# Optimization experiments

Hardware: AMD Instinct MI355X
Metric: run time of the kernel (lower is better)

## Reference

```python
import jax, jax.numpy as jnp
import numpy as np

D_MODEL = 1024
N_LAYERS = 2
D_STATE = 64
D_CONV = 4
EXPAND = 2
D_INNER = EXPAND * D_MODEL            # 2048
HEADDIM = D_STATE                     # 64 (headdim=d_state per module code)
NHEADS = D_INNER // HEADDIM           # 32
CONV_DIM = D_INNER + 2 * D_STATE      # 2176 (ngroups=1)
D_IN_PROJ = 2 * D_INNER + 2 * D_STATE + NHEADS  # 4256
EPS = 1e-5


def setup_inputs() -> dict:
    key = jax.random.key(0)
    ks = jax.random.split(key, 8)
    B, L = 2, 4096
    return {
        "x": jax.random.normal(ks[0], (B, L, D_MODEL), jnp.float32),
        "ln_w": jnp.ones((N_LAYERS, D_MODEL), jnp.float32),
        "ln_b": jnp.zeros((N_LAYERS, D_MODEL), jnp.float32),
        "in_proj_w": jax.random.normal(ks[1], (N_LAYERS, D_IN_PROJ, D_MODEL), jnp.float32) * (D_MODEL ** -0.5),
        "conv_w": jax.random.normal(ks[2], (N_LAYERS, CONV_DIM, D_CONV), jnp.float32) * (D_CONV ** -0.5),
        "conv_b": jnp.zeros((N_LAYERS, CONV_DIM), jnp.float32),
        "dt_bias": jax.random.normal(ks[3], (N_LAYERS, NHEADS), jnp.float32) * 0.5,
        "A_log": jnp.log(jax.random.uniform(ks[4], (N_LAYERS, NHEADS), jnp.float32, 1.0, 16.0)),
        "D": jnp.ones((N_LAYERS, NHEADS), jnp.float32),
        "rms_w": jnp.ones((N_LAYERS, D_INNER), jnp.float32),
        "out_proj_w": jax.random.normal(ks[5], (N_LAYERS, D_MODEL, D_INNER), jnp.float32) * (D_INNER ** -0.5),
    }


def _layernorm(x, w, b):
    m = x.mean(-1, keepdims=True)
    v = ((x - m) ** 2).mean(-1, keepdims=True)
    return (x - m) * jax.lax.rsqrt(v + EPS) * w + b


def _mamba2(u, in_w, conv_w, conv_b, dt_bias, A_log, Dp, rms_w, out_w):
    b, l, _ = u.shape
    zxbcdt = u @ in_w.T                                   # (b,l,D_IN_PROJ)
    z, xBC, dt = jnp.split(zxbcdt, [D_INNER, D_INNER + CONV_DIM], axis=-1)
    dt = jax.nn.softplus(dt + dt_bias)                    # (b,l,H)
    # causal depthwise conv over sequence
    xBC = jnp.transpose(xBC, (0, 2, 1))                   # (b,C,l)
    xBC = jax.lax.conv_general_dilated(
        xBC, conv_w[:, None, :], (1,), [(D_CONV - 1, 0)],
        dimension_numbers=("NCH", "OIH", "NCH"), feature_group_count=CONV_DIM)
    xBC = jnp.transpose(xBC, (0, 2, 1)) + conv_b
    xBC = jax.nn.silu(xBC)
    xh, Bm, Cm = jnp.split(xBC, [D_INNER, D_INNER + D_STATE], axis=-1)
    xh = xh.reshape(b, l, NHEADS, HEADDIM)                # (b,l,H,P)
    A = -jnp.exp(A_log)                                   # (H,)
    dA = jnp.exp(dt * A)                                  # (b,l,H)

    def step(state, inputs):
        dA_t, dt_t, x_t, B_t, C_t = inputs                # (b,H),(b,H),(b,H,P),(b,N),(b,N)
        state = dA_t[:, :, None, None] * state + (dt_t[:, :, None] * x_t)[..., None] * B_t[:, None, None, :]
        y_t = jnp.einsum("bhpn,bn->bhp", state, C_t)
        return state, y_t

    xs = (jnp.moveaxis(dA, 1, 0), jnp.moveaxis(dt, 1, 0), jnp.moveaxis(xh, 1, 0),
          jnp.moveaxis(Bm, 1, 0), jnp.moveaxis(Cm, 1, 0))
    init = jnp.zeros((b, NHEADS, HEADDIM, D_STATE), u.dtype)
    _, ys = jax.lax.scan(step, init, xs)                  # ys: (l,b,H,P)
    y = jnp.moveaxis(ys, 0, 1) + Dp[None, None, :, None] * xh
    y = y.reshape(b, l, D_INNER)
    # gated RMSNorm (norm_before_gate=False): gate then rmsnorm
    y = y * jax.nn.silu(z)
    y = y * jax.lax.rsqrt(jnp.mean(y * y, -1, keepdims=True) + EPS) * rms_w
    return y @ out_w.T


def reference(x, ln_w, ln_b, in_proj_w, conv_w, conv_b, dt_bias, A_log, D, rms_w, out_proj_w):
    h = x
    for i in range(N_LAYERS):
        res = h
        h = _layernorm(h, ln_w[i], ln_b[i])
        h = _mamba2(h, in_proj_w[i], conv_w[i], conv_b[i], dt_bias[i], A_log[i], D[i], rms_w[i], out_proj_w[i])
        h = h + res
    return h
```

## Files before the change

kernel.cpp:

```cpp
#include <hip/hip_runtime.h>
#include <stdint.h>

#define D_MODEL   1024
#define D_STATE   64
#define D_INNER   2048
#define NHEADS    32
#define CONV_DIM  2176
#define D_IN_PROJ 4256
#define NPAD1     4352
#define LSEQ      4096
#define BL        8192
#define NCHUNK    32
#define TCH       128
#define EPS       1e-5f

typedef __attribute__((ext_vector_type(8))) _Float16 f16x8;
typedef __attribute__((ext_vector_type(4))) _Float16 f16x4;
typedef __attribute__((ext_vector_type(4))) float f32x4;

__device__ __forceinline__ void load_lds16(const void* g, void* l) {
  __builtin_amdgcn_global_load_lds((const __attribute__((address_space(1))) void*)g,
                                   (__attribute__((address_space(3))) void*)l, 16, 0, 0);
}

__global__ __launch_bounds__(256) void cvt_w1_kernel(const float* __restrict__ w,
                                                     _Float16* __restrict__ o) {
  size_t idx = (size_t)blockIdx.x * 256 + threadIdx.x;
  int k = idx & 1023;
  size_t nr = idx >> 10;
  int layer = (int)(nr / NPAD1);
  int n = (int)(nr % NPAD1);
  float v = (n < D_IN_PROJ) ? w[((size_t)layer * D_IN_PROJ + n) * 1024 + k] : 0.f;
  o[idx] = (_Float16)v;
}
__global__ __launch_bounds__(256) void cvt_w2_kernel(const float* __restrict__ w,
                                                     _Float16* __restrict__ o) {
  size_t idx = (size_t)blockIdx.x * 256 + threadIdx.x;
  o[idx] = (_Float16)w[idx];
}

__global__ __launch_bounds__(256) void ln_kernel(const float* __restrict__ x,
                                                 const float* __restrict__ w,
                                                 const float* __restrict__ b,
                                                 _Float16* __restrict__ o) {
  int row = blockIdx.x, tid = threadIdx.x;
  const float* xr = x + (size_t)row * D_MODEL;
  float4 v = *(const float4*)(xr + tid * 4);
  float s = v.x + v.y + v.z + v.w;
  float q = v.x * v.x + v.y * v.y + v.z * v.z + v.w * v.w;
  for (int off = 1; off < 64; off <<= 1) { s += __shfl_xor(s, off); q += __shfl_xor(q, off); }
  __shared__ float rs[4], rq[4];
  int wave = tid >> 6, lane = tid & 63;
  if (lane == 0) { rs[wave] = s; rq[wave] = q; }
  __syncthreads();
  s = rs[0] + rs[1] + rs[2] + rs[3];
  q = rq[0] + rq[1] + rq[2] + rq[3];
  float mean = s * (1.f / D_MODEL);
  float var = q * (1.f / D_MODEL) - mean * mean;
  float rstd = rsqrtf(var + EPS);
  int c = tid * 4;
  f16x4 ov;
  ov[0] = (_Float16)((v.x - mean) * rstd * w[c + 0] + b[c + 0]);
  ov[1] = (_Float16)((v.y - mean) * rstd * w[c + 1] + b[c + 1]);
  ov[2] = (_Float16)((v.z - mean) * rstd * w[c + 2] + b[c + 2]);
  ov[3] = (_Float16)((v.w - mean) * rstd * w[c + 3] + b[c + 3]);
  *(f16x4*)(o + (size_t)row * D_MODEL + c) = ov;
}

template <int MODE>
__global__ __launch_bounds__(512, 4) void gemm_f16_kernel(
    const _Float16* __restrict__ A, int lda,
    const _Float16* __restrict__ Bw, int K, int NBN,
    _Float16* __restrict__ Zb, _Float16* __restrict__ XPRE, float* __restrict__ AUX,
    float* __restrict__ Cf, const float* __restrict__ resid) {
  __shared__ _Float16 lA[3][256 * 32];
  __shared__ _Float16 lB[3][128 * 32];
  int tid = threadIdx.x;
  int wv = tid >> 6, lane = tid & 63;
  int nwg = gridDim.x;
  int cpx = nwg >> 3;
  int wg = ((int)blockIdx.x & 7) * cpx + ((int)blockIdx.x >> 3);
  int band = wg / (4 * NBN), rem = wg % (4 * NBN);
  int bm = band * 4 + (rem & 3);
  int bn = rem >> 2;

  const int wm = (wv >> 1) * 64, wn = (wv & 1) * 64;
  const int fr = lane & 15;
  const int s4 = lane >> 4;
  size_t aoff = (size_t)(bm * 256) * lda;
  size_t boff = (size_t)(bn * 128) * K;

  f32x4 acc[4][4];
  f32x4 zero = {0.f, 0.f, 0.f, 0.f};
#pragma unroll
  for (int i = 0; i < 4; ++i)
#pragma unroll
    for (int j = 0; j < 4; ++j) acc[i][j] = zero;

  auto stage = [&](int k0, int buf) {
#pragma unroll
    for (int c = 0; c < 2; ++c) {
      int row = (wv * 2 + c) * 16 + (lane >> 2);
      int col = k0 + (((lane & 3) ^ ((row >> 1) & 3)) << 3);
      load_lds16(A + aoff + (size_t)row * lda + col,
                 &lA[buf][(wv * 2 + c) * 512 + lane * 8]);
    }
    int rowb = wv * 16 + (lane >> 2);
    int colb = k0 + (((lane & 3) ^ ((rowb >> 1) & 3)) << 3);
    load_lds16(Bw + boff + (size_t)rowb * K + colb, &lB[buf][wv * 512 + lane * 8]);
  };

  int nk = K >> 5;
  stage(0, 0);
  stage(32, 1);
  int cur = 0;
  for (int kk = 0; kk < nk; ++kk) {
    if (kk + 2 < nk) {
      int sb = cur + 2; if (sb >= 3) sb -= 3;
      stage((kk + 2) << 5, sb);
      asm volatile("s_waitcnt vmcnt(6)" ::: "memory");
    } else if (kk + 1 < nk) {
      asm volatile("s_waitcnt vmcnt(3)" ::: "memory");
    } else {
      asm volatile("s_waitcnt vmcnt(0)" ::: "memory");
    }
    __builtin_amdgcn_s_barrier();
    __builtin_amdgcn_sched_barrier(0);
    f16x8 af[4], bf[4];
#pragma unroll
    for (int i = 0; i < 4; ++i) {
      int R = wm + i * 16 + fr;
      af[i] = *(const f16x8*)&lA[cur][R * 32 + ((s4 ^ ((R >> 1) & 3)) << 3)];
    }
#pragma unroll
    for (int j = 0; j < 4; ++j) {
      int R = wn + j * 16 + fr;
      bf[j] = *(const f16x8*)&lB[cur][R * 32 + ((s4 ^ ((R >> 1) & 3)) << 3)];
    }
#pragma unroll
    for (int i = 0; i < 4; ++i)
#pragma unroll
      for (int j = 0; j < 4; ++j)
        acc[i][j] = __builtin_amdgcn_mfma_f32_16x16x32_f16(af[i], bf[j], acc[i][j], 0, 0, 0);
    __builtin_amdgcn_sched_barrier(0);
    __builtin_amdgcn_s_barrier();
    cur = cur + 1; if (cur >= 3) cur = 0;
  }

  int r0 = (lane >> 4) * 4;
  int cc = lane & 15;
#pragma unroll
  for (int i = 0; i < 4; ++i) {
#pragma unroll
    for (int j = 0; j < 4; ++j) {
      int col = bn * 128 + wn + j * 16 + cc;
#pragma unroll
      for (int r = 0; r < 4; ++r) {
        size_t row = (size_t)(bm * 256 + wm + i * 16 + r0 + r);
        float v = acc[i][j][r];
        if constexpr (MODE == 0) {
          if (col < 2048)       Zb[row * 2048 + col] = (_Float16)v;
          else if (col < 4096)  XPRE[row * 2048 + (col - 2048)] = (_Float16)v;
          else if (col < 4256)  AUX[row * 160 + (col - 4096)] = v;
        } else {
          size_t idx = row * 1024 + col;
          Cf[idx] = v + resid[idx];
        }
      }
    }
  }
}

__global__ __launch_bounds__(128) void dtlc_kernel(const float* __restrict__ aux,
                                                   const float* __restrict__ dtb,
                                                   const float* __restrict__ alog,
                                                   float* __restrict__ dtt,
                                                   float* __restrict__ lco) {
  int bid = blockIdx.x;
  int h = bid >> 6, b = (bid >> 5) & 1, ct = bid & 31;
  int tid = threadIdx.x, lane = tid & 63;
  int l = b * LSEQ + ct * TCH + tid;
  float A = -__expf(alog[h]);
  float v = aux[(size_t)l * 160 + 128 + h] + dtb[h];
  float sp = (v > 20.f) ? v : log1pf(expf(v));
  size_t base = (size_t)h * BL + b * LSEQ + ct * TCH;
  dtt[base + tid] = sp;
  float d = sp * A;
#pragma unroll
  for (int off = 1; off < 64; off <<= 1) {
    float o = __shfl_up(d, off);
    if (lane >= off) d += o;
  }
  __shared__ float tot;
  if (tid == 63) tot = d;
  __syncthreads();
  if (tid >= 64) d += tot;
  lco[base + tid] = d;
}

__global__ __launch_bounds__(256) void conv_kernel(const _Float16* __restrict__ xpre,
                                                   const float* __restrict__ aux,
                                                   const float* __restrict__ cw,
                                                   const float* __restrict__ cb,
                                                   _Float16* __restrict__ xt,
                                                   float* __restrict__ Bo,
                                                   float* __restrict__ Co,
                                                   _Float16* __restrict__ bt) {
  int c = blockIdx.y * 256 + threadIdx.x;
  if (c >= CONV_DIM) return;
  int l0 = blockIdx.x * 16;
  float w0 = cw[c * 4 + 0], w1 = cw[c * 4 + 1], w2 = cw[c * 4 + 2], w3 = cw[c * 4 + 3];
  float bias = cb[c];
  bool isx = (c < 2048);
  auto ldx = [&](int l) -> float {
    return isx ? (float)xpre[(size_t)l * 2048 + c] : aux[(size_t)l * 160 + (c - 2048)];
  };
  float a0 = 0.f, a1 = 0.f, a2 = 0.f;
  if ((l0 & 4095) != 0) { a0 = ldx(l0 - 3); a1 = ldx(l0 - 2); a2 = ldx(l0 - 1); }
  _Float16 ob[16];
#pragma unroll
  for (int t = 0; t < 16; ++t) {
    int l = l0 + t;
    float a3 = ldx(l);
    float acc = bias + a0 * w0 + a1 * w1 + a2 * w2 + a3 * w3;
    acc = acc / (1.f + __expf(-acc));
    ob[t] = (_Float16)acc;
    if (!isx) {
      if (c < 2112) Bo[(size_t)l * 64 + (c - 2048)] = acc;
      else          Co[(size_t)l * 64 + (c - 2112)] = acc;
    }
    a0 = a1; a1 = a2; a2 = a3;
  }
  f16x8 v0, v1;
#pragma unroll
  for (int j = 0; j < 8; ++j) { v0[j] = ob[j]; v1[j] = ob[8 + j]; }
  if (isx) {
    *(f16x8*)&xt[(size_t)c * 8192 + l0] = v0;
    *(f16x8*)&xt[(size_t)c * 8192 + l0 + 8] = v1;
  } else if (c < 2112) {
    *(f16x8*)&bt[(size_t)(c - 2048) * 8192 + l0] = v0;
    *(f16x8*)&bt[(size_t)(c - 2048) * 8192 + l0 + 8] = v1;
  }
}

__global__ __launch_bounds__(256) void scan_state_kernel(
    const _Float16* __restrict__ xt, const _Float16* __restrict__ bt,
    const float* __restrict__ lc, const float* __restrict__ dtt,
    float* __restrict__ cs) {
  int bid = blockIdx.x;
  int chunk = bid & 31, h = (bid >> 5) & 31, b = bid >> 10;
  int tid = threadIdx.x;
  size_t gb = (size_t)b * LSEQ + chunk * TCH;
  size_t cdb = (size_t)h * BL + gb;
  __shared__ _Float16 xtl[64 * 128];
  __shared__ _Float16 btl[64 * 128];
  __shared__ float ldsW[128];
  if (tid < 128) ldsW[tid] = dtt[cdb + tid] * __expf(lc[cdb + 127] - lc[cdb + tid]);
  __syncthreads();
  int rr = tid >> 4, cl = tid & 15;
#pragma unroll
  for (int p = 0; p < 4; ++p) {
    int row = p * 16 + rr;
    f16x8 v = *(const f16x8*)&xt[(size_t)(h * 64 + row) * BL + gb + cl * 8];
    f16x8 bv = *(const f16x8*)&bt[(size_t)row * BL + gb + cl * 8];
    f16x8 sv;
#pragma unroll
    for (int j = 0; j < 8; ++j) sv[j] = (_Float16)((float)v[j] * ldsW[cl * 8 + j]);
    int byo = (row * 256 + cl * 16) ^ ((row & 7) << 4);
    *(f16x8*)((char*)xtl + byo) = sv;
    *(f16x8*)((char*)btl + byo) = bv;
  }
  __syncthreads();
  int wv = tid >> 6, lane = tid & 63;
  int fr = lane & 15, fk = (lane >> 4) * 8, r0 = (lane >> 4) * 4, cc = lane & 15;
  int swz = (fr & 7) << 4;
  f32x4 acc[4];
  f32x4 zero = {0.f, 0.f, 0.f, 0.f};
#pragma unroll
  for (int j = 0; j < 4; ++j) acc[j] = zero;
#pragma unroll
  for (int k0 = 0; k0 < 128; k0 += 32) {
    f16x8 af = *(const f16x8*)((char*)xtl + (((wv * 16 + fr) * 256 + (k0 + fk) * 2) ^ swz));
#pragma unroll
    for (int j = 0; j < 4; ++j) {
      f16x8 bf = *(const f16x8*)((char*)btl + (((j * 16 + fr) * 256 + (k0 + fk) * 2) ^ swz));
      acc[j] = __builtin_amdgcn_mfma_f32_16x16x32_f16(af, bf, acc[j], 0, 0, 0);
    }
  }
  size_t cbase = (((size_t)(b * 32 + h) * 32) + chunk) * 4096;
#pragma unroll
  for (int j = 0; j < 4; ++j)
#pragma unroll
    for (int r = 0; r < 4; ++r)
      cs[cbase + (wv * 16 + r0 + r) * 64 + j * 16 + cc] = acc[j][r];
}

__global__ __launch_bounds__(256) void scan_p2_kernel(float* __restrict__ cs,
                                                      const float* __restrict__ lc) {
  int bid = blockIdx.x;
  int b = bid >> 7, h = (bid >> 2) & 31, pq = bid & 3;
  int tid = threadIdx.x;
  size_t base = ((size_t)(b * 32 + h) * 32) * 4096 + (size_t)(pq * 256 + tid) * 4;
  const float* lcd = lc + (size_t)h * BL + b * LSEQ;
  float4 s = {0.f, 0.f, 0.f, 0.f};
  for (int c = 0; c < NCHUNK; ++c) {
    size_t idx = base + (size_t)c * 4096;
    float4 e = *(const float4*)&cs[idx];
    float P = __expf(lcd[c * TCH + TCH - 1]);
    *(float4*)&cs[idx] = s;
    s.x = e.x + P * s.x;
    s.y = e.y + P * s.y;
    s.z = e.z + P * s.z;
    s.w = e.w + P * s.w;
  }
}

__global__ __launch_bounds__(256) void scan_y_kernel(
    const _Float16* __restrict__ xt, const float* __restrict__ Cc,
    const float* __restrict__ Bc, const float* __restrict__ cs,
    const float* __restrict__ lc, const float* __restrict__ dtt,
    const float* __restrict__ Dv, _Float16* __restrict__ y) {
  int bid = blockIdx.x;
  int chunk = bid & 31, h = (bid >> 5) & 31, b = bid >> 10;
  int tid = threadIdx.x;
  size_t gb = (size_t)b * LSEQ + chunk * TCH;
  size_t cdb = (size_t)h * BL + gb;

  __shared__ _Float16 uCB[2 * 128 * 64];
  __shared__ _Float16 xtl[64 * 128];
  __shared__ _Float16 spl[64 * 64];
  __shared__ float ldsLc[128];
  __shared__ float ldsDt[128];
  _Float16* Cl = uCB;
  _Float16* Bl = uCB + 128 * 64;
  _Float16* Pl = uCB;

  int rr = tid >> 4, cl = tid & 15;
#pragma unroll
  for (int p = 0; p < 8; ++p) {
    int row = p * 16 + rr;
    float4 cv = *(const float4*)&Cc[(gb + row) * 64 + cl * 4];
    float4 bv = *(const float4*)&Bc[(gb + row) * 64 + cl * 4];
    f16x4 ch = {(_Float16)cv.x, (_Float16)cv.y, (_Float16)cv.z, (_Float16)cv.w};
    f16x4 bh = {(_Float16)bv.x, (_Float16)bv.y, (_Float16)bv.z, (_Float16)bv.w};
    int byo = (row * 128 + cl * 8) ^ ((row & 7) << 4);
    *(f16x4*)((char*)Cl + byo) = ch;
    *(f16x4*)((char*)Bl + byo) = bh;
  }
  size_t cbase = (((size_t)(b * 32 + h) * 32) + chunk) * 4096;
#pragma unroll
  for (int p = 0; p < 4; ++p) {
    int row = p * 16 + rr;
    f16x8 v = *(const f16x8*)&xt[(size_t)(h * 64 + row) * BL + gb + cl * 8];
    int byo = (row * 256 + cl * 16) ^ ((row & 7) << 4);
    *(f16x8*)((char*)xtl + byo) = v;
    float4 sv = *(const float4*)&cs[cbase + row * 64 + cl * 4];
    f16x4 sh = {(_Float16)sv.x, (_Float16)sv.y, (_Float16)sv.z, (_Float16)sv.w};
    int byo2 = (row * 128 + cl * 8) ^ ((row & 7) << 4);
    *(f16x4*)((char*)spl + byo2) = sh;
  }
  if (tid < 128) { ldsLc[tid] = lc[cdb + tid]; ldsDt[tid] = dtt[cdb + tid]; }
  __syncthreads();

  int wv = tid >> 6, lane = tid & 63;
  int fr = lane & 15, fk = (lane >> 4) * 8, r0 = (lane >> 4) * 4, cc = lane & 15;
  int tb = wv * 32;
  int swz = (fr & 7) << 4;

  f32x4 accY[2][4];
  f32x4 accS[2][8];
  f32x4 zero = {0.f, 0.f, 0.f, 0.f};
#pragma unroll
  for (int i = 0; i < 2; ++i) {
#pragma unroll
    for (int j = 0; j < 4; ++j) accY[i][j] = zero;
#pragma unroll
    for (int j = 0; j < 8; ++j) accS[i][j] = zero;
  }

#pragma unroll
  for (int k0 = 0; k0 < 64; k0 += 32) {
    f16x8 ac[2];
#pragma unroll
    for (int i = 0; i < 2; ++i)
      ac[i] = *(const f16x8*)((char*)Cl + (((tb + i * 16 + fr) * 128 + (k0 + fk) * 2) ^ swz));
#pragma unroll
    for (int j = 0; j < 4; ++j) {
      f16x8 bs = *(const f16x8*)((char*)spl + (((j * 16 + fr) * 128 + (k0 + fk) * 2) ^ swz));
#pragma unroll
      for (int i = 0; i < 2; ++i)
        accY[i][j] = __builtin_amdgcn_mfma_f32_16x16x32_f16(ac[i], bs, accY[i][j], 0, 0, 0);
    }
#pragma unroll
    for (int j = 0; j < 8; ++j) {
      f16x8 bb = *(const f16x8*)((char*)Bl + (((j * 16 + fr) * 128 + (k0 + fk) * 2) ^ swz));
#pragma unroll
      for (int i = 0; i < 2; ++i)
        accS[i][j] = __builtin_amdgcn_mfma_f32_16x16x32_f16(ac[i], bb, accS[i][j], 0, 0, 0);
    }
  }

  float lct[2][4];
#pragma unroll
  for (int i = 0; i < 2; ++i)
#pragma unroll
    for (int r = 0; r < 4; ++r) lct[i][r] = ldsLc[tb + i * 16 + r0 + r];
#pragma unroll
  for (int i = 0; i < 2; ++i)
#pragma unroll
    for (int r = 0; r < 4; ++r) {
      float sc = __expf(lct[i][r]);
#pragma unroll
      for (int j = 0; j < 4; ++j) accY[i][j][r] *= sc;
    }

  __syncthreads();
  float Dh = Dv[h];
#pragma unroll
  for (int i = 0; i < 2; ++i)
#pragma unroll
    for (int jj = 0; jj < 8; ++jj) {
      int s = jj * 16 + cc;
      float lcs = ldsLc[s];
      float dts = ldsDt[s];
#pragma unroll
      for (int r = 0; r < 4; ++r) {
        int t = tb + i * 16 + r0 + r;
        float v = 0.f;
        if (s <= t) v = accS[i][jj][r] * __expf(lct[i][r] - lcs) * dts;
        if (s == t) v += Dh;
        int byo = (t * 256 + s * 2) ^ ((t & 7) << 4);
        *(_Float16*)((char*)Pl + byo) = (_Float16)v;
      }
    }
  __syncthreads();

#pragma unroll
  for (int k0 = 0; k0 < 128; k0 += 32) {
    f16x8 ap[2];
#pragma unroll
    for (int i = 0; i < 2; ++i)
      ap[i] = *(const f16x8*)((char*)Pl + (((tb + i * 16 + fr) * 256 + (k0 + fk) * 2) ^ swz));
#pragma unroll
    for (int j = 0; j < 4; ++j) {
      f16x8 bx = *(const f16x8*)((char*)xtl + (((j * 16 + fr) * 256 + (k0 + fk) * 2) ^ swz));
#pragma unroll
      for (int i = 0; i < 2; ++i)
        accY[i][j] = __builtin_amdgcn_mfma_f32_16x16x32_f16(ap[i], bx, accY[i][j], 0, 0, 0);
    }
  }

#pragma unroll
  for (int i = 0; i < 2; ++i)
#pragma unroll
    for (int j = 0; j < 4; ++j)
#pragma unroll
      for (int r = 0; r < 4; ++r) {
        int t = tb + i * 16 + r0 + r;
        y[(gb + t) * 2048 + h * 64 + j * 16 + cc] = (_Float16)accY[i][j][r];
      }
}

__global__ __launch_bounds__(256) void gate_rms_kernel(const _Float16* __restrict__ yf,
                                                       const _Float16* __restrict__ zb,
                                                       const float* __restrict__ rw,
                                                       _Float16* __restrict__ g) {
  int row = blockIdx.x, tid = threadIdx.x;
  int c0 = tid * 8;
  f16x8 yv = *(const f16x8*)(yf + (size_t)row * D_INNER + c0);
  f16x8 zv = *(const f16x8*)(zb + (size_t)row * D_INNER + c0);
  float gv[8];
  float q = 0.f;
#pragma unroll
  for (int u = 0; u < 8; ++u) {
    float yy = (float)yv[u];
    float zz = (float)zv[u];
    float t = yy * (zz / (1.f + __expf(-zz)));
    gv[u] = t;
    q += t * t;
  }
  for (int off = 1; off < 64; off <<= 1) q += __shfl_xor(q, off);
  __shared__ float rq[4];
  if ((tid & 63) == 0) rq[tid >> 6] = q;
  __syncthreads();
  q = rq[0] + rq[1] + rq[2] + rq[3];
  float scale = rsqrtf(q * (1.f / D_INNER) + EPS);
  float4 r0 = *(const float4*)&rw[c0];
  float4 r1 = *(const float4*)&rw[c0 + 4];
  f16x8 o;
  o[0] = (_Float16)(gv[0] * scale * r0.x);
  o[1] = (_Float16)(gv[1] * scale * r0.y);
  o[2] = (_Float16)(gv[2] * scale * r0.z);
  o[3] = (_Float16)(gv[3] * scale * r0.w);
  o[4] = (_Float16)(gv[4] * scale * r1.x);
  o[5] = (_Float16)(gv[5] * scale * r1.y);
  o[6] = (_Float16)(gv[6] * scale * r1.z);
  o[7] = (_Float16)(gv[7] * scale * r1.w);
  *(f16x8*)(g + (size_t)row * D_INNER + c0) = o;
}

extern "C" void kernel_launch(void* const* d_in, const int* in_sizes, int n_in,
                              void* d_out, int out_size, void* d_ws, size_t ws_size,
                              hipStream_t stream) {
  (void)in_sizes; (void)n_in; (void)out_size; (void)ws_size;
  const float* x     = (const float*)d_in[0];
  const float* ln_w  = (const float*)d_in[1];
  const float* ln_b  = (const float*)d_in[2];
  const float* w_in  = (const float*)d_in[3];
  const float* cw    = (const float*)d_in[4];
  const float* cb    = (const float*)d_in[5];
  const float* dtb   = (const float*)d_in[6];
  const float* alog  = (const float*)d_in[7];
  const float* dvec  = (const float*)d_in[8];
  const float* rmsw  = (const float*)d_in[9];
  const float* w_out = (const float*)d_in[10];
  float* out = (float*)d_out;

  char* ws = (char*)d_ws;
  size_t off = 0;
  auto alloc = [&](size_t bytes) -> char* {
    char* p = ws + off;
    off += (bytes + 255) & ~(size_t)255;
    return p;
  };
  _Float16* W1 = (_Float16*)alloc(2ull * 2 * NPAD1 * 1024);
  _Float16* W2 = (_Float16*)alloc(2ull * 2 * 1024 * 2048);
  char* REGION = alloc(4ull * BL * D_INNER);
  _Float16* LNf = (_Float16*)REGION;
  _Float16* Yf = (_Float16*)REGION;
  _Float16* Zb = (_Float16*)alloc(2ull * BL * D_INNER);
  _Float16* XPRE = (_Float16*)alloc(2ull * BL * D_INNER);
  _Float16* XT = (_Float16*)alloc(2ull * BL * D_INNER);
  float* AUX  = (float*)alloc(4ull * BL * 160);
  float* BC = (float*)alloc(4ull * BL * D_STATE);
  float* CC = (float*)alloc(4ull * BL * D_STATE);
  float* DTt = (float*)alloc(4ull * NHEADS * BL);
  float* LC  = (float*)alloc(4ull * NHEADS * BL);
  _Float16* BT = (_Float16*)alloc(2ull * D_STATE * BL);
  float* CS = (float*)alloc(4ull * 2 * NHEADS * NCHUNK * 4096);

  cvt_w1_kernel<<<(2 * NPAD1 * 1024) / 256, 256, 0, stream>>>(w_in, W1);
  cvt_w2_kernel<<<(2 * 1024 * 2048) / 256, 256, 0, stream>>>(w_out, W2);

  for (int layer = 0; layer < 2; ++layer) {
    const float* hin = layer ? (const float*)out : x;
    size_t o1 = (size_t)layer * NPAD1 * 1024;
    size_t o2 = (size_t)layer * 1024 * 2048;
    ln_kernel<<<BL, 256, 0, stream>>>(hin, ln_w + layer * D_MODEL, ln_b + layer * D_MODEL, LNf);
    gemm_f16_kernel<0><<<dim3((8192 / 256) * (NPAD1 / 128)), 512, 0, stream>>>(
        LNf, 1024, W1 + o1, 1024, NPAD1 / 128, Zb, XPRE, AUX, nullptr, nullptr);
    dtlc_kernel<<<2048, 128, 0, stream>>>(AUX, dtb + layer * NHEADS,
                                          alog + layer * NHEADS, DTt, LC);
    conv_kernel<<<dim3(BL / 16, 9), 256, 0, stream>>>(XPRE, AUX, cw + layer * CONV_DIM * 4,
                                                      cb + layer * CONV_DIM, XT, BC, CC, BT);
    scan_state_kernel<<<2048, 256, 0, stream>>>(XT, BT, LC, DTt, CS);
    scan_p2_kernel<<<256, 256, 0, stream>>>(CS, LC);
    scan_y_kernel<<<2048, 256, 0, stream>>>(XT, CC, BC, CS, LC, DTt,
                                            dvec + layer * NHEADS, Yf);
    gate_rms_kernel<<<BL, 256, 0, stream>>>(Yf, Zb, rmsw + layer * D_INNER, Zb);
    gemm_f16_kernel<1><<<dim3((8192 / 256) * (1024 / 128)), 512, 0, stream>>>(
        Zb, 2048, W2 + o2, 2048, 1024 / 128, nullptr, nullptr, nullptr, out, hin);
  }
}
```

Before: 743.7 us.

## Make GEMMs persistent over tiles and pack conv B/C output as fp16

Both GEMM launches now use a fixed grid (512 and 256 workgroups) that loops over output tiles, keeping the per-XCD tile grouping so each workgroup handles several tiles in turn. Separately, the conv kernel writes B and C as a single interleaved fp16 buffer instead of two fp32 arrays, so scan_y can load them with one 16-byte read and skip its conversion step. The persistent loop is meant to cut launch and tail overhead and improve cache locality, but it changes occupancy and wave balance (1088 tiles over 512 workgroups does not divide evenly). The fp16 B/C buffer halves that memory traffic.

```diff
diff --git a/kernel.cpp b/kernel.cpp
--- a/kernel.cpp
+++ b/kernel.cpp
@@ -70,101 +70,105 @@
 template <int MODE>
 __global__ __launch_bounds__(512, 4) void gemm_f16_kernel(
     const _Float16* __restrict__ A, int lda,
-    const _Float16* __restrict__ Bw, int K, int NBN,
+    const _Float16* __restrict__ Bw, int K, int NBN, int NT,
     _Float16* __restrict__ Zb, _Float16* __restrict__ XPRE, float* __restrict__ AUX,
     float* __restrict__ Cf, const float* __restrict__ resid) {
   __shared__ _Float16 lA[3][256 * 32];
   __shared__ _Float16 lB[3][128 * 32];
   int tid = threadIdx.x;
   int wv = tid >> 6, lane = tid & 63;
-  int nwg = gridDim.x;
-  int cpx = nwg >> 3;
-  int wg = ((int)blockIdx.x & 7) * cpx + ((int)blockIdx.x >> 3);
-  int band = wg / (4 * NBN), rem = wg % (4 * NBN);
-  int bm = band * 4 + (rem & 3);
-  int bn = rem >> 2;
-
   const int wm = (wv >> 1) * 64, wn = (wv & 1) * 64;
   const int fr = lane & 15;
   const int s4 = lane >> 4;
-  size_t aoff = (size_t)(bm * 256) * lda;
-  size_t boff = (size_t)(bn * 128) * K;
-
-  f32x4 acc[4][4];
-  f32x4 zero = {0.f, 0.f, 0.f, 0.f};
-#pragma unroll
-  for (int i = 0; i < 4; ++i)
-#pragma unroll
-    for (int j = 0; j < 4; ++j) acc[i][j] = zero;
-
-  auto stage = [&](int k0, int buf) {
-#pragma unroll
-    for (int c = 0; c < 2; ++c) {
-      int row = (wv * 2 + c) * 16 + (lane >> 2);
-      int col = k0 + (((lane & 3) ^ ((row >> 1) & 3)) << 3);
-      load_lds16(A + aoff + (size_t)row * lda + col,
-                 &lA[buf][(wv * 2 + c) * 512 + lane * 8]);
-    }
-    int rowb = wv * 16 + (lane >> 2);
-    int colb = k0 + (((lane & 3) ^ ((rowb >> 1) & 3)) << 3);
-    load_lds16(Bw + boff + (size_t)rowb * K + colb, &lB[buf][wv * 512 + lane * 8]);
-  };
-
-  int nk = K >> 5;
-  stage(0, 0);
-  stage(32, 1);
-  int cur = 0;
-  for (int kk = 0; kk < nk; ++kk) {
-    if (kk + 2 < nk) {
-      int sb = cur + 2; if (sb >= 3) sb -= 3;
-      stage((kk + 2) << 5, sb);
-      asm volatile("s_waitcnt vmcnt(6)" ::: "memory");
-    } else if (kk + 1 < nk) {
-      asm volatile("s_waitcnt vmcnt(3)" ::: "memory");
-    } else {
-      asm volatile("s_waitcnt vmcnt(0)" ::: "memory");
-    }
-    __builtin_amdgcn_s_barrier();
-    __builtin_amdgcn_sched_barrier(0);
-    f16x8 af[4], bf[4];
+  int nwg = gridDim.x;
+  int cpt = NT >> 3;
+  int xcd = (int)blockIdx.x & 7;
+  int step = nwg >> 3;
+
+  for (int lt = (int)blockIdx.x >> 3; lt < cpt; lt += step) {
+    int wg = xcd * cpt + lt;
+    int band = wg / (4 * NBN), rem = wg % (4 * NBN);
+    int bm = band * 4 + (rem & 3);
+    int bn = rem >> 2;
+    size_t aoff = (size_t)(bm * 256) * lda;
+    size_t boff = (size_t)(bn * 128) * K;
+
+    f32x4 acc[4][4];
+    f32x4 zero = {0.f, 0.f, 0.f, 0.f};
+#pragma unroll
+    for (int i = 0; i < 4; ++i)
+#pragma unroll
+      for (int j = 0; j < 4; ++j) acc[i][j] = zero;
+
+    auto stage = [&](int k0, int buf) {
+#pragma unroll
+      for (int c = 0; c < 2; ++c) {
+        int row = (wv * 2 + c) * 16 + (lane >> 2);
+        int col = k0 + (((lane & 3) ^ ((row >> 1) & 3)) << 3);
+        load_lds16(A + aoff + (size_t)row * lda + col,
+                   &lA[buf][(wv * 2 + c) * 512 + lane * 8]);
+      }
+      int rowb = wv * 16 + (lane >> 2);
+      int colb = k0 + (((lane & 3) ^ ((rowb >> 1) & 3)) << 3);
+      load_lds16(Bw + boff + (size_t)rowb * K + colb, &lB[buf][wv * 512 + lane * 8]);
+    };
+
+    int nk = K >> 5;
+    stage(0, 0);
+    stage(32, 1);
+    int cur = 0;
+    for (int kk = 0; kk < nk; ++kk) {
+      if (kk + 2 < nk) {
+        int sb = cur + 2; if (sb >= 3) sb -= 3;
+        stage((kk + 2) << 5, sb);
+        asm volatile("s_waitcnt vmcnt(6)" ::: "memory");
+      } else if (kk + 1 < nk) {
+        asm volatile("s_waitcnt vmcnt(3)" ::: "memory");
+      } else {
+        asm volatile("s_waitcnt vmcnt(0)" ::: "memory");
+      }
+      __builtin_amdgcn_s_barrier();
+      __builtin_amdgcn_sched_barrier(0);
+      f16x8 af[4], bf[4];
+#pragma unroll
+      for (int i = 0; i < 4; ++i) {
+        int R = wm + i * 16 + fr;
+        af[i] = *(const f16x8*)&lA[cur][R * 32 + ((s4 ^ ((R >> 1) & 3)) << 3)];
+      }
+#pragma unroll
+      for (int j = 0; j < 4; ++j) {
+        int R = wn + j * 16 + fr;
+        bf[j] = *(const f16x8*)&lB[cur][R * 32 + ((s4 ^ ((R >> 1) & 3)) << 3)];
+      }
+#pragma unroll
+      for (int i = 0; i < 4; ++i)
+#pragma unroll
+        for (int j = 0; j < 4; ++j)
+          acc[i][j] = __builtin_amdgcn_mfma_f32_16x16x32_f16(af[i], bf[j], acc[i][j], 0, 0, 0);
+      __builtin_amdgcn_sched_barrier(0);
+      __builtin_amdgcn_s_barrier();
+      cur = cur + 1; if (cur >= 3) cur = 0;
+    }
+
+    int r0 = (lane >> 4) * 4;
+    int cc = lane & 15;
 #pragma unroll
     for (int i = 0; i < 4; ++i) {
-      int R = wm + i * 16 + fr;
-      af[i] = *(const f16x8*)&lA[cur][R * 32 + ((s4 ^ ((R >> 1) & 3)) << 3)];
-    }
-#pragma unroll
-    for (int j = 0; j < 4; ++j) {
-      int R = wn + j * 16 + fr;
-      bf[j] = *(const f16x8*)&lB[cur][R * 32 + ((s4 ^ ((R >> 1) & 3)) << 3)];
-    }
-#pragma unroll
-    for (int i = 0; i < 4; ++i)
-#pragma unroll
-      for (int j = 0; j < 4; ++j)
-        acc[i][j] = __builtin_amdgcn_mfma_f32_16x16x32_f16(af[i], bf[j], acc[i][j], 0, 0, 0);
-    __builtin_amdgcn_sched_barrier(0);
-    __builtin_amdgcn_s_barrier();
-    cur = cur + 1; if (cur >= 3) cur = 0;
-  }
-
-  int r0 = (lane >> 4) * 4;
-  int cc = lane & 15;
-#pragma unroll
-  for (int i = 0; i < 4; ++i) {
-#pragma unroll
-    for (int j = 0; j < 4; ++j) {
-      int col = bn * 128 + wn + j * 16 + cc;
-#pragma unroll
-      for (int r = 0; r < 4; ++r) {
-        size_t row = (size_t)(bm * 256 + wm + i * 16 + r0 + r);
-        float v = acc[i][j][r];
-        if constexpr (MODE == 0) {
-          if (col < 2048)       Zb[row * 2048 + col] = (_Float16)v;
-          else if (col < 4096)  XPRE[row * 2048 + (col - 2048)] = (_Float16)v;
-          else if (col < 4256)  AUX[row * 160 + (col - 4096)] = v;
-        } else {
-          size_t idx = row * 1024 + col;
-          Cf[idx] = v + resid[idx];
+#pragma unroll
+      for (int j = 0; j < 4; ++j) {
+        int col = bn * 128 + wn + j * 16 + cc;
+#pragma unroll
+        for (int r = 0; r < 4; ++r) {
+          size_t row = (size_t)(bm * 256 + wm + i * 16 + r0 + r);
+          float v = acc[i][j][r];
+          if constexpr (MODE == 0) {
+            if (col < 2048)       Zb[row * 2048 + col] = (_Float16)v;
+            else if (col < 4096)  XPRE[row * 2048 + (col - 2048)] = (_Float16)v;
+            else if (col < 4256)  AUX[row * 160 + (col - 4096)] = v;
+          } else {
+            size_t idx = row * 1024 + col;
+            Cf[idx] = v + resid[idx];
+          }
         }
       }
     }
@@ -203,8 +207,7 @@
                                                    const float* __restrict__ cw,
                                                    const float* __restrict__ cb,
                                                    _Float16* __restrict__ xt,
-                                                   float* __restrict__ Bo,
-                                                   float* __restrict__ Co,
+                                                   _Float16* __restrict__ cbh,
                                                    _Float16* __restrict__ bt) {
   int c = blockIdx.y * 256 + threadIdx.x;
   if (c >= CONV_DIM) return;
@@ -225,10 +228,7 @@
     float acc = bias + a0 * w0 + a1 * w1 + a2 * w2 + a3 * w3;
     acc = acc / (1.f + __expf(-acc));
     ob[t] = (_Float16)acc;
-    if (!isx) {
-      if (c < 2112) Bo[(size_t)l * 64 + (c - 2048)] = acc;
-      else          Co[(size_t)l * 64 + (c - 2112)] = acc;
-    }
+    if (!isx) cbh[(size_t)l * 128 + (c - 2048)] = ob[t];
     a0 = a1; a1 = a2; a2 = a3;
   }
   f16x8 v0, v1;
@@ -316,10 +316,10 @@
 }
 
 __global__ __launch_bounds__(256) void scan_y_kernel(
-    const _Float16* __restrict__ xt, const float* __restrict__ Cc,
-    const float* __restrict__ Bc, const float* __restrict__ cs,
-    const float* __restrict__ lc, const float* __restrict__ dtt,
-    const float* __restrict__ Dv, _Float16* __restrict__ y) {
+    const _Float16* __restrict__ xt, const _Float16* __restrict__ cbh,
+    const float* __restrict__ cs, const float* __restrict__ lc,
+    const float* __restrict__ dtt, const float* __restrict__ Dv,
+    _Float16* __restrict__ y) {
   int bid = blockIdx.x;
   int chunk = bid & 31, h = (bid >> 5) & 31, b = bid >> 10;
   int tid = threadIdx.x;
@@ -339,13 +339,10 @@
 #pragma unroll
   for (int p = 0; p < 8; ++p) {
     int row = p * 16 + rr;
-    float4 cv = *(const float4*)&Cc[(gb + row) * 64 + cl * 4];
-    float4 bv = *(const float4*)&Bc[(gb + row) * 64 + cl * 4];
-    f16x4 ch = {(_Float16)cv.x, (_Float16)cv.y, (_Float16)cv.z, (_Float16)cv.w};
-    f16x4 bh = {(_Float16)bv.x, (_Float16)bv.y, (_Float16)bv.z, (_Float16)bv.w};
-    int byo = (row * 128 + cl * 8) ^ ((row & 7) << 4);
-    *(f16x4*)((char*)Cl + byo) = ch;
-    *(f16x4*)((char*)Bl + byo) = bh;
+    f16x8 v = *(const f16x8*)&cbh[(gb + row) * 128 + cl * 8];
+    int byo = (row * 128 + (cl & 7) * 16) ^ ((row & 7) << 4);
+    if (cl < 8) *(f16x8*)((char*)Bl + byo) = v;
+    else        *(f16x8*)((char*)Cl + byo) = v;
   }
   size_t cbase = (((size_t)(b * 32 + h) * 32) + chunk) * 4096;
 #pragma unroll
@@ -532,8 +529,7 @@
   _Float16* XPRE = (_Float16*)alloc(2ull * BL * D_INNER);
   _Float16* XT = (_Float16*)alloc(2ull * BL * D_INNER);
   float* AUX  = (float*)alloc(4ull * BL * 160);
-  float* BC = (float*)alloc(4ull * BL * D_STATE);
-  float* CC = (float*)alloc(4ull * BL * D_STATE);
+  _Float16* CB16 = (_Float16*)alloc(2ull * BL * 128);
   float* DTt = (float*)alloc(4ull * NHEADS * BL);
   float* LC  = (float*)alloc(4ull * NHEADS * BL);
   _Float16* BT = (_Float16*)alloc(2ull * D_STATE * BL);
@@ -547,18 +543,20 @@
     size_t o1 = (size_t)layer * NPAD1 * 1024;
     size_t o2 = (size_t)layer * 1024 * 2048;
     ln_kernel<<<BL, 256, 0, stream>>>(hin, ln_w + layer * D_MODEL, ln_b + layer * D_MODEL, LNf);
-    gemm_f16_kernel<0><<<dim3((8192 / 256) * (NPAD1 / 128)), 512, 0, stream>>>(
-        LNf, 1024, W1 + o1, 1024, NPAD1 / 128, Zb, XPRE, AUX, nullptr, nullptr);
+    gemm_f16_kernel<0><<<512, 512, 0, stream>>>(
+        LNf, 1024, W1 + o1, 1024, NPAD1 / 128, (8192 / 256) * (NPAD1 / 128),
+        Zb, XPRE, AUX, nullptr, nullptr);
     dtlc_kernel<<<2048, 128, 0, stream>>>(AUX, dtb + layer * NHEADS,
                                           alog + layer * NHEADS, DTt, LC);
     conv_kernel<<<dim3(BL / 16, 9), 256, 0, stream>>>(XPRE, AUX, cw + layer * CONV_DIM * 4,
-                                                      cb + layer * CONV_DIM, XT, BC, CC, BT);
+                                                      cb + layer * CONV_DIM, XT, CB16, BT);
     scan_state_kernel<<<2048, 256, 0, stream>>>(XT, BT, LC, DTt, CS);
     scan_p2_kernel<<<256, 256, 0, stream>>>(CS, LC);
-    scan_y_kernel<<<2048, 256, 0, stream>>>(XT, CC, BC, CS, LC, DTt,
+    scan_y_kernel<<<2048, 256, 0, stream>>>(XT, CB16, CS, LC, DTt,
                                             dvec + layer * NHEADS, Yf);
     gate_rms_kernel<<<BL, 256, 0, stream>>>(Yf, Zb, rmsw + layer * D_INNER, Zb);
-    gemm_f16_kernel<1><<<dim3((8192 / 256) * (1024 / 128)), 512, 0, stream>>>(
-        Zb, 2048, W2 + o2, 2048, 1024 / 128, nullptr, nullptr, nullptr, out, hin);
-  }
-}
+    gemm_f16_kernel<1><<<256, 512, 0, stream>>>(
+        Zb, 2048, W2 + o2, 2048, 1024 / 128, (8192 / 256) * (1024 / 128),
+        nullptr, nullptr, nullptr, out, hin);
+  }
+}
```

Measured after the change: 760.1 us. 1.02x slower.
